# Performance work log

Hardware: AMD Instinct MI355X
Metric: run time of the kernel (lower is better)

Reference implementation:

```python
import jax, jax.numpy as jnp
import numpy as np
from jax.scipy.special import gammaln, logsumexp

N, P, K, R = 100000, 256, 64, 16

def setup_inputs() -> dict:
    key = jax.random.key(0)
    kx, km, kp = jax.random.split(key, 3)
    X = jax.random.normal(kx, (N, P), dtype=jnp.float32)
    X = X / jnp.linalg.norm(X, axis=1, keepdims=True)  # points on the sphere S^{p-1}
    M = jax.random.normal(km, (K, P, R), dtype=jnp.float32)
    pi = jax.random.normal(kp, (K,), dtype=jnp.float32)
    return {"X": X, "M": M, "pi": pi}

def reference(X, M, pi):
    p = X.shape[1]
    r = M.shape[-1]
    half_p = 0.5 * float(p)
    # log surface area constant of the ACG normalizer
    logSA = gammaln(half_p) - jnp.log(2.0) - half_p * jnp.log(jnp.pi)
    # D = I_r + M^T M per component: [K, r, r]
    D = jnp.eye(r, dtype=M.dtype) + jnp.einsum('kpr,kps->krs', M, M)
    _, log_det_D = jnp.linalg.slogdet(D)            # [K]
    Dinv = jnp.linalg.inv(D)                        # [K, r, r]
    XM = jnp.einsum('np,kpr->knr', X, M)            # [K, N, r]
    quad = jnp.einsum('knr,krs,kns->kn', XM, Dinv, XM)  # [K, N]
    pdf = 1.0 - quad                                # Woodbury: x^T Sigma^{-1} x for unit x
    log_acg_pdf = logSA - 0.5 * log_det_D[:, None] - half_p * jnp.log(pdf)
    density = log_acg_pdf + jax.nn.log_softmax(pi)[:, None]   # [K, N]
    loglik = jnp.sum(logsumexp(density, axis=0))
    return loglik
```

## Files before the change

kernel.cpp:

```cpp
#include <hip/hip_runtime.h>
#include <hip/hip_bf16.h>
#include <math.h>

#define NPTS 100000
#define NSTRIPE 1568
#define KCOMP 64

typedef float v4f __attribute__((ext_vector_type(4)));
typedef __bf16 v8bf __attribute__((ext_vector_type(8)));
typedef __bf16 v4bf __attribute__((ext_vector_type(4)));


__global__ __launch_bounds__(256) void prep_comp(const float* __restrict__ M,
                                                 const float* __restrict__ pi,
                                                 __bf16* __restrict__ Bt,
                                                 float* __restrict__ cvec,
                                                 float logSA) {
    __shared__ float Ml[256][16];
    __shared__ float S[16][17];
    __shared__ float sh_logpi;
    const int k = blockIdx.x, t = threadIdx.x;

    const float4* src = (const float4*)(M + (size_t)k * 4096 + (size_t)t * 16);
    float4 a0 = src[0], a1 = src[1], a2 = src[2], a3 = src[3];
    ((float4*)Ml[t])[0] = a0; ((float4*)Ml[t])[1] = a1;
    ((float4*)Ml[t])[2] = a2; ((float4*)Ml[t])[3] = a3;

    if (t < 64) {
        float v = pi[t];
        float mx = v;
        for (int off = 32; off; off >>= 1) mx = fmaxf(mx, __shfl_xor(mx, off));
        float e = __expf(v - mx);
        float s = e;
        for (int off = 32; off; off >>= 1) s += __shfl_xor(s, off);
        if (t == 0) sh_logpi = pi[k] - mx - logf(s);
    }
    __syncthreads();

    {
        int r = t >> 4, c = t & 15;
        float s = (r == c) ? 1.0f : 0.0f;
        for (int p = 0; p < 256; ++p) s += Ml[p][r] * Ml[p][c];
        S[r][c] = s;
    }
    __syncthreads();

    for (int j = 0; j < 16; ++j) {
        if (t == 0) S[j][j] = sqrtf(S[j][j]);
        __syncthreads();
        if (t > j && t < 16) S[t][j] = S[t][j] / S[j][j];
        __syncthreads();
        {
            int r = t >> 4, c = t & 15;
            if (r > j && c > j && c <= r) S[r][c] -= S[r][j] * S[c][j];
        }
        __syncthreads();
    }

    if (t == 0) {
        float ldet = 0.0f;
        for (int j = 0; j < 16; ++j) ldet += logf(S[j][j]);
        cvec[k] = logSA - ldet + sh_logpi;
    }

    float m[16] = {a0.x, a0.y, a0.z, a0.w, a1.x, a1.y, a1.z, a1.w,
                   a2.x, a2.y, a2.z, a2.w, a3.x, a3.y, a3.z, a3.w};
    float y[16];
#pragma unroll
    for (int r = 0; r < 16; ++r) {
        float v = m[r];
#pragma unroll
        for (int q = 0; q < r; ++q) v -= S[r][q] * y[q];
        y[r] = v / S[r][r];
    }
    const int cw = k >> 2, n = k & 3;
    const int ks = t >> 5, e = t & 7;
    const int lbase = ((t >> 3) & 3) * 16;
#pragma unroll
    for (int r = 0; r < 16; ++r) {
        const size_t off = (size_t)cw * 16384 + (size_t)ks * 2048 + (size_t)n * 512
                         + (size_t)(lbase + r) * 8 + e;
        Bt[off] = (__bf16)y[r];
    }
}

__global__ __launch_bounds__(256) void convert_X(const float* __restrict__ X,
                                                 __bf16* __restrict__ Xb) {
    __shared__ __bf16 T[64][264];
    const int st = blockIdx.x;
    const int n0 = st * 64;
    const int t = threadIdx.x;

#pragma unroll
    for (int j = 0; j < 16; ++j) {
        const int u = j * 256 + t;
        const int r = u >> 6, c4 = u & 63;
        const int n = n0 + r;
        float4 v = make_float4(0.f, 0.f, 0.f, 0.f);
        if (n < NPTS) v = ((const float4*)X)[(size_t)n * 64 + c4];
        v4bf o = {(__bf16)v.x, (__bf16)v.y, (__bf16)v.z, (__bf16)v.w};
        *(v4bf*)&T[r][c4 * 4] = o;
    }
    __syncthreads();

#pragma unroll
    for (int ks = 0; ks < 8; ++ks) {
        const int mh = t >> 6;
        const int l = t & 63;
        const int row = mh * 16 + (l & 15);
        const int col = ks * 32 + (l >> 4) * 8;
        v8bf val = *(const v8bf*)&T[row][col];
        const size_t off = (size_t)st * 16384 + (size_t)ks * 2048
                         + (size_t)mh * 512 + (size_t)l * 8;
        *(v8bf*)(Xb + off) = val;
    }
}

__global__ __launch_bounds__(512, 2) void gemm_density(const __bf16* __restrict__ Xb,
                                                       const __bf16* __restrict__ Bt,
                                                       const float* __restrict__ cvec,
                                                       float* __restrict__ out) {
    __shared__ float psum[8][4][16][2];
    const int bid = blockIdx.x;
    const int xcd = bid & 7, i = bid >> 3;
    const int st = xcd * 196 + i;
    const int t = threadIdx.x;
    const int w = t >> 6, lane = t & 63;
    const int lo = lane & 15;
    const int n0 = st * 64;
    const int cw0 = w << 1;

    const __bf16* Ab = Xb + ((size_t)st << 14) + lane * 8;
    const __bf16* Bb = Bt + lane * 8;

#define LOADB(dst, cw_, ks_) do {                                          \
    const __bf16* _p = Bb + ((size_t)(cw_) << 14) + ((size_t)(ks_) << 11); \
    dst[0] = *(const v8bf*)(_p);                                           \
    dst[1] = *(const v8bf*)(_p + 512);                                     \
    dst[2] = *(const v8bf*)(_p + 1024);                                    \
    dst[3] = *(const v8bf*)(_p + 1536);                                    \
} while (0)

    v8bf bg[4][4];
    LOADB(bg[0], cw0, 0);
    LOADB(bg[1], cw0, 1);
    LOADB(bg[2], cw0, 2);

    float mrun[4] = {-INFINITY, -INFINITY, -INFINITY, -INFINITY};
    float srun[4] = {0.f, 0.f, 0.f, 0.f};
    const float4* cv4 = (const float4*)cvec;

#pragma unroll 1
    for (int c = 0; c < 2; ++c) {
        const int cw = cw0 + c;
        const int cwn = cw0 + ((c + 1) & 1);
        v4f acc[4][4] = {};
#pragma unroll
        for (int ks = 0; ks < 8; ++ks) {
            const int pk = ks + 3;
            const int pcw = (pk < 8) ? cw : cwn;
            LOADB(bg[pk & 3], pcw, pk & 7);
            v8bf af[4];
#pragma unroll
            for (int m = 0; m < 4; ++m)
                af[m] = *(const v8bf*)(Ab + ks * 2048 + m * 512);
#pragma unroll
            for (int m = 0; m < 4; ++m)
#pragma unroll
                for (int n = 0; n < 4; ++n)
                    acc[m][n] = __builtin_amdgcn_mfma_f32_16x16x32_bf16(
                        bg[ks & 3][n], af[m], acc[m][n], 0, 0, 0);
        }

        const float4 cv = cv4[cw];
#pragma unroll
        for (int m = 0; m < 4; ++m) {
            float d[4];
#pragma unroll
            for (int n = 0; n < 4; ++n) {
                v4f qv = acc[m][n];
                float s = qv[0] * qv[0] + qv[1] * qv[1] + qv[2] * qv[2] + qv[3] * qv[3];
                s += __shfl_xor(s, 16);
                s += __shfl_xor(s, 32);
                const float cc = (n == 0) ? cv.x : (n == 1) ? cv.y : (n == 2) ? cv.z : cv.w;
                d[n] = cc - 128.0f * __logf(1.0f - s);
            }
            const float mt = fmaxf(fmaxf(d[0], d[1]), fmaxf(d[2], d[3]));
            const float mn = fmaxf(mrun[m], mt);
            srun[m] = srun[m] * __expf(mrun[m] - mn)
                    + __expf(d[0] - mn) + __expf(d[1] - mn)
                    + __expf(d[2] - mn) + __expf(d[3] - mn);
            mrun[m] = mn;
        }
    }
#undef LOADB

    if (lane < 16) {
#pragma unroll
        for (int m = 0; m < 4; ++m) {
            psum[w][m][lo][0] = mrun[m];
            psum[w][m][lo][1] = srun[m];
        }
    }
    __syncthreads();
    if (t < 64) {
        const int m = t >> 4, l = t & 15;
        float M0 = psum[0][m][l][0];
#pragma unroll
        for (int q = 1; q < 8; ++q) M0 = fmaxf(M0, psum[q][m][l][0]);
        float s = 0.f;
#pragma unroll
        for (int q = 0; q < 8; ++q)
            s += psum[q][m][l][1] * __expf(psum[q][m][l][0] - M0);
        const int pt = n0 + t;
        float local = (pt < NPTS) ? (M0 + __logf(s)) : 0.f;
        for (int off = 32; off; off >>= 1) local += __shfl_xor(local, off);
        if (t == 0) atomicAdd(out, local);
    }
}

extern "C" void kernel_launch(void* const* d_in, const int* in_sizes, int n_in,
                              void* d_out, int out_size, void* d_ws, size_t ws_size,
                              hipStream_t stream) {
    const float* X  = (const float*)d_in[0];
    const float* M  = (const float*)d_in[1];
    const float* pi = (const float*)d_in[2];
    float* out = (float*)d_out;

    char* ws = (char*)d_ws;
    __bf16* Xb   = (__bf16*)ws;
    __bf16* Bt   = (__bf16*)(ws + 51380224);
    float*  cvec = (float*)(ws + 51904512);

    const double half_p = 128.0;
    const float logSA = (float)(lgamma(half_p) - log(2.0) - half_p * log(M_PI));

    hipMemsetAsync(d_out, 0, sizeof(float), stream);
    prep_comp<<<64, 256, 0, stream>>>(M, pi, Bt, cvec, logSA);
    convert_X<<<NSTRIPE, 256, 0, stream>>>(X, Xb);
    gemm_density<<<NSTRIPE, 512, 0, stream>>>(Xb, Bt, cvec, out);
}
```

Measured before the change: 129.6 us.

## Repartition GEMM warps into 2x2 row/component tiles with 256-thread blocks

The gemm_density block shrinks from 8 waves to 4. Each wave now covers 32 rows and 8 component groups (32 components) instead of 64 rows and 2 component groups. The reuse of each B fragment across rows halves while the reuse of A across components grows, and the cross-wave logsumexp merge is reduced to two partials. The launch bound moves to 3 blocks per CU, aiming at better occupancy and less redundant B traffic per block, at the cost of a longer serial loop per wave.

```diff
diff --git a/kernel.cpp b/kernel.cpp
--- a/kernel.cpp
+++ b/kernel.cpp
@@ -116,21 +116,22 @@
     }
 }
 
-__global__ __launch_bounds__(512, 2) void gemm_density(const __bf16* __restrict__ Xb,
+__global__ __launch_bounds__(256, 3) void gemm_density(const __bf16* __restrict__ Xb,
                                                        const __bf16* __restrict__ Bt,
                                                        const float* __restrict__ cvec,
                                                        float* __restrict__ out) {
-    __shared__ float psum[8][4][16][2];
+    __shared__ float psum[4][2][16][2];
     const int bid = blockIdx.x;
     const int xcd = bid & 7, i = bid >> 3;
     const int st = xcd * 196 + i;
     const int t = threadIdx.x;
     const int w = t >> 6, lane = t & 63;
     const int lo = lane & 15;
+    const int mh = w >> 1, cq = w & 1;
     const int n0 = st * 64;
-    const int cw0 = w << 1;
-
-    const __bf16* Ab = Xb + ((size_t)st << 14) + lane * 8;
+    const int cw0 = cq << 3;
+
+    const __bf16* Ab = Xb + ((size_t)st << 14) + (size_t)mh * 1024 + lane * 8;
     const __bf16* Bb = Bt + lane * 8;
 
 #define LOADB(dst, cw_, ks_) do {                                          \
@@ -146,26 +147,25 @@
     LOADB(bg[1], cw0, 1);
     LOADB(bg[2], cw0, 2);
 
-    float mrun[4] = {-INFINITY, -INFINITY, -INFINITY, -INFINITY};
-    float srun[4] = {0.f, 0.f, 0.f, 0.f};
+    float mrun[2] = {-INFINITY, -INFINITY};
+    float srun[2] = {0.f, 0.f};
     const float4* cv4 = (const float4*)cvec;
 
 #pragma unroll 1
-    for (int c = 0; c < 2; ++c) {
+    for (int c = 0; c < 8; ++c) {
         const int cw = cw0 + c;
-        const int cwn = cw0 + ((c + 1) & 1);
-        v4f acc[4][4] = {};
+        const int cwn = cw0 + ((c + 1) & 7);
+        v4f acc[2][4] = {};
 #pragma unroll
         for (int ks = 0; ks < 8; ++ks) {
             const int pk = ks + 3;
             const int pcw = (pk < 8) ? cw : cwn;
             LOADB(bg[pk & 3], pcw, pk & 7);
-            v8bf af[4];
-#pragma unroll
-            for (int m = 0; m < 4; ++m)
-                af[m] = *(const v8bf*)(Ab + ks * 2048 + m * 512);
-#pragma unroll
-            for (int m = 0; m < 4; ++m)
+            v8bf af[2];
+            af[0] = *(const v8bf*)(Ab + ks * 2048);
+            af[1] = *(const v8bf*)(Ab + ks * 2048 + 512);
+#pragma unroll
+            for (int m = 0; m < 2; ++m)
 #pragma unroll
                 for (int n = 0; n < 4; ++n)
                     acc[m][n] = __builtin_amdgcn_mfma_f32_16x16x32_bf16(
@@ -174,7 +174,7 @@
 
         const float4 cv = cv4[cw];
 #pragma unroll
-        for (int m = 0; m < 4; ++m) {
+        for (int m = 0; m < 2; ++m) {
             float d[4];
 #pragma unroll
             for (int n = 0; n < 4; ++n) {
@@ -197,22 +197,21 @@
 
     if (lane < 16) {
 #pragma unroll
-        for (int m = 0; m < 4; ++m) {
+        for (int m = 0; m < 2; ++m) {
             psum[w][m][lo][0] = mrun[m];
             psum[w][m][lo][1] = srun[m];
         }
     }
     __syncthreads();
     if (t < 64) {
-        const int m = t >> 4, l = t & 15;
-        float M0 = psum[0][m][l][0];
-#pragma unroll
-        for (int q = 1; q < 8; ++q) M0 = fmaxf(M0, psum[q][m][l][0]);
-        float s = 0.f;
-#pragma unroll
-        for (int q = 0; q < 8; ++q)
-            s += psum[q][m][l][1] * __expf(psum[q][m][l][0] - M0);
-        const int pt = n0 + t;
+        const int r = t;
+        const int mh_ = r >> 5, m_ = (r >> 4) & 1, l = r & 15;
+        const int w0 = 2 * mh_, w1 = 2 * mh_ + 1;
+        const float a0 = psum[w0][m_][l][0], a1 = psum[w0][m_][l][1];
+        const float b0 = psum[w1][m_][l][0], b1 = psum[w1][m_][l][1];
+        const float M0 = fmaxf(a0, b0);
+        const float s = a1 * __expf(a0 - M0) + b1 * __expf(b0 - M0);
+        const int pt = n0 + r;
         float local = (pt < NPTS) ? (M0 + __logf(s)) : 0.f;
         for (int off = 32; off; off >>= 1) local += __shfl_xor(local, off);
         if (t == 0) atomicAdd(out, local);
@@ -238,5 +237,5 @@
     hipMemsetAsync(d_out, 0, sizeof(float), stream);
     prep_comp<<<64, 256, 0, stream>>>(M, pi, Bt, cvec, logSA);
     convert_X<<<NSTRIPE, 256, 0, stream>>>(X, Xb);
-    gemm_density<<<NSTRIPE, 512, 0, stream>>>(Xb, Bt, cvec, out);
-}
+    gemm_density<<<NSTRIPE, 256, 0, stream>>>(Xb, Bt, cvec, out);
+}
```

Measured after the change: 136.3 us. 5.2% more time.
